# Kernel tuning notes

Hardware: AMD Instinct MI355X
Metric: run time of the kernel (lower is better)

The kernel has to match this reference:

```python
import jax, jax.numpy as jnp
import numpy as np

B, T, C = 1, 2048, 1024
E = 32            # n_routed_experts
TOPK = 4
H = 512           # expert_hidden_size
HS = 1024         # shared hidden: round_up(2*512, 256)
ROUTE_SCALE = 1.0


def setup_inputs() -> dict:
    key = jax.random.key(0)
    ks = jax.random.split(key, 6)
    s = 0.02  # init scale for stable logits/activations
    return {
        "x": jax.random.normal(ks[0], (B, T, C), jnp.float32),
        "gate_w": jax.random.normal(ks[1], (C, E), jnp.float32) * s,
        "gate_bias": jnp.zeros((E,), jnp.float32),
        "shared_gate_w": jax.random.normal(ks[2], (C, 2 * HS), jnp.float32) * s,
        "shared_down_w": jax.random.normal(ks[3], (HS, C), jnp.float32) * s,
        "expert_gate_w": jax.random.normal(ks[4], (E, C, 2 * H), jnp.float32) * s,
        "expert_down_w": jax.random.normal(ks[5], (E, H, C), jnp.float32) * s,
    }


def _swiglu(x, gate_w, down_w):
    # torch: y, gate = chunk(gate_proj(x), 2); down(silu(gate) * y)
    u = x @ gate_w
    y, g = jnp.split(u, 2, axis=-1)
    return (jax.nn.silu(g) * y) @ down_w


def reference(x, gate_w, gate_bias, shared_gate_w, shared_down_w,
              expert_gate_w, expert_down_w):
    Bx, Tx, Cx = x.shape
    xf = x.reshape(-1, Cx)                     # (N, C)
    N = xf.shape[0]

    # shared expert (always active)
    shared = _swiglu(x, shared_gate_w, shared_down_w)   # (B, T, C)

    # sigmoid top-k gate with load-balance bias (bias only affects selection)
    scores = jax.nn.sigmoid(xf @ gate_w)                # (N, E)
    _, topk_idx = jax.lax.top_k(scores + gate_bias, TOPK)
    w = jnp.take_along_axis(scores, topk_idx, axis=-1)  # (N, K)
    w = w / jnp.sum(w, axis=-1, keepdims=True) * ROUTE_SCALE

    # dense combine weights: combine[n, e] = routing weight of expert e for token n (0 if unselected)
    combine = jnp.zeros((N, E), xf.dtype).at[jnp.arange(N)[:, None], topk_idx].add(w)

    # routed experts: masked dense evaluation (math identical to permute + grouped GEMM + scatter-combine)
    out = jnp.zeros_like(xf)
    for e in range(E):
        out = out + combine[:, e:e + 1] * _swiglu(xf, expert_gate_w[e], expert_down_w[e])

    return shared + out.reshape(Bx, Tx, Cx)
```

## Files before the change

### kernel.cpp

```cpp
#include <hip/hip_runtime.h>
#include <hip/hip_bf16.h>
#include <math.h>

#define N_TOK 2048
#define C_DIM 1024
#define E_NUM 32
#define TOPKK 4
#define H_EXP 512
#define HS_SH 1024
#define NSLOT (N_TOK * TOPKK)

typedef __attribute__((ext_vector_type(8))) short short8;
typedef __attribute__((ext_vector_type(4))) float f32x4;

__device__ __forceinline__ ushort f2b(float f) {
    __hip_bfloat16 h = __float2bfloat16(f);
    return *(ushort*)&h;
}
__device__ __forceinline__ float silu_f(float g) { return g / (1.f + __expf(-g)); }

__device__ __forceinline__ void glds16(const ushort* g, ushort* l) {
    __builtin_amdgcn_global_load_lds(
        (const __attribute__((address_space(1))) unsigned int*)g,
        (__attribute__((address_space(3))) unsigned int*)l, 16, 0, 0);
}

__device__ __forceinline__ void router_body(
    int n, int t, const float* __restrict__ x, const float* __restrict__ gate_w,
    const float* __restrict__ gate_bias, ushort* __restrict__ xb,
    int* __restrict__ topk_idx, float* __restrict__ topk_w, char* smem)
{
    float* xs = (float*)smem;
    float (*part)[E_NUM] = (float(*)[E_NUM])(smem + 4096);
    float* scores_s = (float*)(smem + 4096 + 1024);
    const float* xr = x + (size_t)n * C_DIM;
    {
        float4 v = ((const float4*)xr)[t];
        xs[t * 4 + 0] = v.x; xs[t * 4 + 1] = v.y;
        xs[t * 4 + 2] = v.z; xs[t * 4 + 3] = v.w;
        ushort4 o;
        o.x = f2b(v.x); o.y = f2b(v.y); o.z = f2b(v.z); o.w = f2b(v.w);
        ((ushort4*)(xb + (size_t)n * C_DIM))[t] = o;
    }
    __syncthreads();
    const int e = t & 31, cp = t >> 5;
    float s = 0.f;
#pragma unroll 4
    for (int c = cp * 128; c < cp * 128 + 128; ++c)
        s += xs[c] * gate_w[c * E_NUM + e];
    part[cp][e] = s;
    __syncthreads();
    if (t < E_NUM) {
        float tot = 0.f;
#pragma unroll
        for (int i = 0; i < 8; ++i) tot += part[i][t];
        scores_s[t] = 1.f / (1.f + expf(-tot));
    }
    __syncthreads();
    if (t < 64) {
        const int l = t;
        const float sc  = (l < E_NUM) ? scores_s[l] : -INFINITY;
        const float scb = (l < E_NUM) ? sc + gate_bias[l] : -INFINITY;
        bool used = false;
        int myidx[TOPKK]; float myw[TOPKK]; float wsum = 0.f;
#pragma unroll
        for (int k = 0; k < TOPKK; ++k) {
            float v = used ? -INFINITY : scb;
            float m = v;
#pragma unroll
            for (int d = 1; d < 64; d <<= 1) m = fmaxf(m, __shfl_xor(m, d));
            unsigned long long b = __ballot(v == m);
            const int pick = __ffsll((unsigned long long)b) - 1;
            if (l == pick) used = true;
            const float w = __shfl(sc, pick);
            myidx[k] = pick; myw[k] = w; wsum += w;
        }
        if (l == 0) {
            const float inv = 1.0f / wsum;
#pragma unroll
            for (int k = 0; k < TOPKK; ++k) {
                topk_idx[n * TOPKK + k] = myidx[k];
                topk_w[n * TOPKK + k] = myw[k] * inv;
            }
        }
    }
}

template<int K, int N, int PAIR_H>
__device__ __forceinline__ void transp_body(const float* __restrict__ in,
                                            ushort* __restrict__ out,
                                            int bx, int by, int bz, int t, char* smem)
{
    const float* inp = in + (size_t)bz * K * N;
    ushort* outp = out + (size_t)bz * K * N;
    ushort (*T)[132] = (ushort(*)[132])smem;
    const int k0 = by * 64, n0 = bx * 128;
    {
        const int rr = t >> 5;
        const int c4 = (t & 31) * 4;
        float4 v[8];
#pragma unroll
        for (int i = 0; i < 8; ++i)
            v[i] = *(const float4*)(inp + (size_t)(k0 + rr + i * 8) * N + n0 + c4);
#pragma unroll
        for (int i = 0; i < 8; ++i) {
            const int row = rr + i * 8;
            ushort4 o;
            o.x = f2b(v[i].x); o.y = f2b(v[i].y); o.z = f2b(v[i].z); o.w = f2b(v[i].w);
            *(ushort4*)&T[row][c4 ^ ((row >> 3) << 2)] = o;
        }
    }
    __syncthreads();
    {
        const int g  = t >> 3;
        const int kg = t & 7;
#pragma unroll
        for (int p = 0; p < 4; ++p) {
            const int nn = p * 32 + g;
            const int nsw = nn ^ (kg << 2);
            const int gn = n0 + nn;
            int np;
            if (PAIR_H > 0)
                np = (gn < PAIR_H) ? ((gn >> 4) * 32 + (gn & 15))
                                   : (((gn - PAIR_H) >> 4) * 32 + 16 + ((gn - PAIR_H) & 15));
            else
                np = gn;
            short8 o;
#pragma unroll
            for (int j = 0; j < 8; ++j) o[j] = (short)T[kg * 8 + j][nsw];
            *(short8*)(outp + (size_t)np * K + k0 + kg * 8) = o;
        }
    }
}

__global__ __launch_bounds__(256) void prep_mega(
    const float* __restrict__ x, const float* __restrict__ gw,
    const float* __restrict__ gb, const float* __restrict__ sgw,
    const float* __restrict__ egw, ushort* __restrict__ xb,
    int* __restrict__ topk_idx, float* __restrict__ topk_w,
    ushort* __restrict__ sgw_t, ushort* __restrict__ egw_t)
{
    __shared__ __align__(16) char smem[16896];
    const int b = blockIdx.x;
    const int t = threadIdx.x;
    if (b < 256) {
        transp_body<C_DIM, 2 * HS_SH, HS_SH>(sgw, sgw_t, b & 15, b >> 4, 0, t, smem);
    } else if (b < 4352) {
        const int r = b - 256;
        transp_body<C_DIM, 2 * H_EXP, H_EXP>(egw, egw_t, r & 7, (r >> 3) & 15, r >> 7, t, smem);
    } else {
        router_body(b - 4352, t, x, gw, gb, xb, topk_idx, topk_w, smem);
    }
}

__global__ __launch_bounds__(1024) void route_build(
    const int* __restrict__ topk_idx, const float* __restrict__ topk_w,
    int* __restrict__ offsets, int* __restrict__ perm_token,
    float* __restrict__ perm_w, int* __restrict__ inv_slot)
{
    __shared__ int cnt[E_NUM];
    __shared__ int off_s[E_NUM + 1];
    const int t = threadIdx.x;
    if (t < E_NUM) cnt[t] = 0;
    __syncthreads();
    int myidx[8];
#pragma unroll
    for (int j = 0; j < 8; ++j) {
        const int i = t * 8 + j;
        myidx[j] = topk_idx[i];
        atomicAdd(&cnt[myidx[j]], 1);
    }
    __syncthreads();
    if (t == 0) {
        int a = 0;
        for (int e2 = 0; e2 < E_NUM; ++e2) { off_s[e2] = a; a += cnt[e2]; }
        off_s[E_NUM] = a;
    }
    __syncthreads();
    if (t < E_NUM) cnt[t] = off_s[t];
    if (t <= E_NUM) offsets[t] = off_s[t];
    __syncthreads();
#pragma unroll
    for (int j = 0; j < 8; ++j) {
        const int i = t * 8 + j;
        const int pos = atomicAdd(&cnt[myidx[j]], 1);
        perm_token[pos] = i >> 2;
        perm_w[pos] = topk_w[i];
        inv_slot[i] = pos;
    }
}

template<int K, int NP, bool EXPERT>
__device__ __forceinline__ void swiglu_body(
    const ushort* __restrict__ Ab, const ushort* __restrict__ Bt,
    ushort* __restrict__ Out, const int* __restrict__ offsets,
    const int* __restrict__ perm_tok, int eidx, ushort* S)
{
    constexpr int H = NP / 2;
    int base = 0, cnt = N_TOK;
    const ushort* Bp = Bt;
    if (EXPERT) {
        base = offsets[eidx]; cnt = offsets[eidx + 1] - base;
        Bp = Bt + (size_t)eidx * NP * K;
    }
    const int n0 = blockIdx.x * 128;
    if (n0 >= NP) return;
    const int m0 = blockIdx.y * 128;
    if (m0 >= cnt) return;
    ushort* O = Out + (size_t)base * H;

    ushort* As = S;
    ushort* Bs = S + 128 * 64;

    const int t = threadIdx.x;
    const int lane = t & 63, wave = t >> 6;
    const int wr = wave >> 1, wc = wave & 1;
    const int quad = lane >> 4, l16 = lane & 15;
    const int srow = lane >> 3;
    const int schunk = (lane & 7) ^ srow;

    f32x4 acc[4][4];
#pragma unroll
    for (int i = 0; i < 4; ++i)
#pragma unroll
        for (int j = 0; j < 4; ++j) acc[i][j] = (f32x4){0.f, 0.f, 0.f, 0.f};

    const ushort* AgI[4];
#pragma unroll
    for (int i = 0; i < 4; ++i) {
        int ar = m0 + wave * 8 + srow + i * 32;
        if (EXPERT) {
            ar = ar < cnt ? ar : 0;
            AgI[i] = Ab + (size_t)perm_tok[base + ar] * K + schunk * 8;
        } else {
            AgI[i] = Ab + (size_t)(base + ar) * K + schunk * 8;
        }
    }
    const ushort* Bg = Bp + (size_t)(n0 + wave * 8 + srow) * K + schunk * 8;

    for (int k0 = 0; k0 < K; k0 += 64) {
        __syncthreads();
#pragma unroll
        for (int i = 0; i < 4; ++i) {
            glds16(AgI[i] + k0, As + (wave * 8 + i * 32) * 64);
            glds16(Bg + (size_t)(i * 32) * K + k0, Bs + (wave * 8 + i * 32) * 64);
        }
        __syncthreads();
#pragma unroll
        for (int ks = 0; ks < 2; ++ks) {
            const int coff = (((ks * 4 + quad) ^ (l16 & 7)) << 3);
            short8 af[4], bfr[4];
#pragma unroll
            for (int i = 0; i < 4; ++i) {
                af[i]  = *(const short8*)(As + (wr * 64 + i * 16 + l16) * 64 + coff);
                bfr[i] = *(const short8*)(Bs + (wc * 64 + i * 16 + l16) * 64 + coff);
            }
#pragma unroll
            for (int tm = 0; tm < 4; ++tm)
#pragma unroll
                for (int tn = 0; tn < 4; ++tn)
                    acc[tm][tn] = __builtin_amdgcn_mfma_f32_16x16x32_bf16(
                        af[tm], bfr[tn], acc[tm][tn], 0, 0, 0);
        }
    }

    __syncthreads();
#pragma unroll
    for (int tm = 0; tm < 4; ++tm)
#pragma unroll
        for (int p = 0; p < 2; ++p)
#pragma unroll
            for (int r = 0; r < 4; ++r) {
                const int ml = wr * 64 + tm * 16 + quad * 4 + r;
                const int hl = wc * 32 + p * 16 + l16;
                const float y = acc[tm][2 * p][r];
                const float g = acc[tm][2 * p + 1][r];
                S[ml * 72 + hl] = f2b(silu_f(g) * y);
            }
    __syncthreads();
#pragma unroll
    for (int i = 0; i < 4; ++i) {
        const int c = t + i * 256;
        const int row = c >> 3, col = (c & 7) * 8;
        if (m0 + row < cnt)
            *(float4*)(O + (size_t)(m0 + row) * H + (n0 >> 1) + col) =
                *(const float4*)(S + row * 72 + col);
    }
}

template<int K, bool EXPERT>
__device__ __forceinline__ void down_body(
    const ushort* __restrict__ Ab, const ushort* __restrict__ Bt,
    float* __restrict__ Out, const int* __restrict__ offsets,
    const float* __restrict__ perm_w, int eidx, ushort* S)
{
    int base = 0, cnt = N_TOK;
    const ushort* Bp = Bt;
    if (EXPERT) {
        base = offsets[eidx]; cnt = offsets[eidx + 1] - base;
        Bp = Bt + (size_t)eidx * C_DIM * K;
    }
    const int m0 = blockIdx.y * 128;
    if (m0 >= cnt) return;
    const int n0 = blockIdx.x * 128;
    const ushort* Ap = Ab + (size_t)base * K;

    ushort* As = S;
    ushort* Bs = S + 128 * 64;

    const int t = threadIdx.x;
    const int lane = t & 63, wave = t >> 6;
    const int wr = wave >> 1, wc = wave & 1;
    const int quad = lane >> 4, l16 = lane & 15;
    const int srow = lane >> 3;
    const int schunk = (lane & 7) ^ srow;

    f32x4 acc[4][4];
#pragma unroll
    for (int i = 0; i < 4; ++i)
#pragma unroll
        for (int j = 0; j < 4; ++j) acc[i][j] = (f32x4){0.f, 0.f, 0.f, 0.f};

    const ushort* Ag = Ap + (size_t)(m0 + wave * 8 + srow) * K + schunk * 8;
    const ushort* Bg = Bp + (size_t)(n0 + wave * 8 + srow) * K + schunk * 8;

    for (int k0 = 0; k0 < K; k0 += 64) {
        __syncthreads();
#pragma unroll
        for (int i = 0; i < 4; ++i) {
            glds16(Ag + (size_t)(i * 32) * K + k0, As + (wave * 8 + i * 32) * 64);
            glds16(Bg + (size_t)(i * 32) * K + k0, Bs + (wave * 8 + i * 32) * 64);
        }
        __syncthreads();
#pragma unroll
        for (int ks = 0; ks < 2; ++ks) {
            const int coff = (((ks * 4 + quad) ^ (l16 & 7)) << 3);
            short8 af[4], bfr[4];
#pragma unroll
            for (int i = 0; i < 4; ++i) {
                af[i]  = *(const short8*)(As + (wr * 64 + i * 16 + l16) * 64 + coff);
                bfr[i] = *(const short8*)(Bs + (wc * 64 + i * 16 + l16) * 64 + coff);
            }
#pragma unroll
            for (int tm = 0; tm < 4; ++tm)
#pragma unroll
                for (int tn = 0; tn < 4; ++tn)
                    acc[tm][tn] = __builtin_amdgcn_mfma_f32_16x16x32_bf16(
                        af[tm], bfr[tn], acc[tm][tn], 0, 0, 0);
        }
    }

#pragma unroll
    for (int tm = 0; tm < 4; ++tm)
#pragma unroll
        for (int r = 0; r < 4; ++r) {
            const int grow = m0 + wr * 64 + tm * 16 + quad * 4 + r;
            if (EXPERT) {
                if (grow < cnt) {
                    const float w = perm_w[base + grow];
#pragma unroll
                    for (int tn = 0; tn < 4; ++tn) {
                        const int col = n0 + wc * 64 + tn * 16 + l16;
                        Out[(size_t)(base + grow) * C_DIM + col] = w * acc[tm][tn][r];
                    }
                }
            } else {
#pragma unroll
                for (int tn = 0; tn < 4; ++tn) {
                    const int col = n0 + wc * 64 + tn * 16 + l16;
                    Out[(size_t)grow * C_DIM + col] = acc[tm][tn][r];
                }
            }
        }
}

__global__ __launch_bounds__(256, 3) void swiglu_fused(
    const ushort* __restrict__ xb, const ushort* __restrict__ sgw_t,
    const ushort* __restrict__ egw_t, ushort* __restrict__ Hs_b,
    ushort* __restrict__ He_b, const int* __restrict__ offsets,
    const int* __restrict__ perm_tok,
    const float* __restrict__ sdw, const float* __restrict__ edw,
    ushort* __restrict__ sdw_t, ushort* __restrict__ edw_t)
{
    __shared__ __align__(16) ushort S[2 * 128 * 64];
    const int z = blockIdx.z;
    if (z >= 33) {
        const int flat = (z - 33) * 256 + blockIdx.y * 16 + blockIdx.x;
        if (flat < 128) {
            transp_body<HS_SH, C_DIM, 0>(sdw, sdw_t, flat & 7, flat >> 3, 0,
                                         threadIdx.x, (char*)S);
        } else if (flat < 2176) {
            const int r = flat - 128;
            transp_body<H_EXP, C_DIM, 0>(edw, edw_t, r & 7, (r >> 3) & 7, r >> 6,
                                         threadIdx.x, (char*)S);
        }
        return;
    }
    if (z < E_NUM)
        swiglu_body<C_DIM, 2 * H_EXP, true>(xb, egw_t, He_b, offsets, perm_tok, z, S);
    else
        swiglu_body<C_DIM, 2 * HS_SH, false>(xb, sgw_t, Hs_b, nullptr, nullptr, 0, S);
}

__global__ __launch_bounds__(256, 3) void down_fused(
    const ushort* __restrict__ Hs_b, const ushort* __restrict__ He_b,
    const ushort* __restrict__ sdw_t, const ushort* __restrict__ edw_t,
    float* __restrict__ out, float* __restrict__ Ye,
    const int* __restrict__ offsets, const float* __restrict__ perm_w)
{
    __shared__ __align__(16) ushort S[2 * 128 * 64];
    const int z = blockIdx.z;
    if (z < E_NUM)
        down_body<H_EXP, true>(He_b, edw_t, Ye, offsets, perm_w, z, S);
    else
        down_body<HS_SH, false>(Hs_b, sdw_t, out, nullptr, nullptr, 0, S);
}

__global__ __launch_bounds__(256) void combine_kernel(
    const float* __restrict__ Ye, const int* __restrict__ inv_slot,
    float* __restrict__ Out)
{
    const int tok = blockIdx.x;
    __shared__ int s4[TOPKK];
    if (threadIdx.x < TOPKK) s4[threadIdx.x] = inv_slot[tok * TOPKK + threadIdx.x];
    __syncthreads();
    const int c = threadIdx.x * 4;
    float4 acc = *(const float4*)(Out + (size_t)tok * C_DIM + c);
#pragma unroll
    for (int k = 0; k < TOPKK; ++k) {
        float4 v = *(const float4*)(Ye + (size_t)s4[k] * C_DIM + c);
        acc.x += v.x; acc.y += v.y; acc.z += v.z; acc.w += v.w;
    }
    *(float4*)(Out + (size_t)tok * C_DIM + c) = acc;
}

extern "C" void kernel_launch(void* const* d_in, const int* in_sizes, int n_in,
                              void* d_out, int out_size, void* d_ws, size_t ws_size,
                              hipStream_t stream)
{
    const float* x   = (const float*)d_in[0];
    const float* gw  = (const float*)d_in[1];
    const float* gb  = (const float*)d_in[2];
    const float* sgw = (const float*)d_in[3];
    const float* sdw = (const float*)d_in[4];
    const float* egw = (const float*)d_in[5];
    const float* edw = (const float*)d_in[6];
    float* out = (float*)d_out;

    char* ws = (char*)d_ws;
    size_t off = 0;
    auto alloc = [&](size_t bytes) -> void* {
        void* p = ws + off;
        off = (off + bytes + 255) & ~(size_t)255;
        return p;
    };
    int*    topk_idx = (int*)   alloc((size_t)NSLOT * sizeof(int));
    float*  topk_w   = (float*) alloc((size_t)NSLOT * sizeof(float));
    int*    offsets  = (int*)   alloc((E_NUM + 1) * sizeof(int));
    int*    perm_tok = (int*)   alloc((size_t)NSLOT * sizeof(int));
    float*  perm_w   = (float*) alloc((size_t)NSLOT * sizeof(float));
    int*    inv_slot = (int*)   alloc((size_t)NSLOT * sizeof(int));
    ushort* xb       = (ushort*)alloc((size_t)N_TOK * C_DIM * 2);
    ushort* sgw_t    = (ushort*)alloc((size_t)C_DIM * 2 * HS_SH * 2);
    ushort* sdw_t    = (ushort*)alloc((size_t)HS_SH * C_DIM * 2);
    ushort* egw_t    = (ushort*)alloc((size_t)E_NUM * C_DIM * 2 * H_EXP * 2);
    ushort* edw_t    = (ushort*)alloc((size_t)E_NUM * H_EXP * C_DIM * 2);
    ushort* Hs_b     = (ushort*)alloc((size_t)N_TOK * HS_SH * 2);
    ushort* He_b     = (ushort*)alloc((size_t)(NSLOT + 128) * H_EXP * 2);
    float*  Ye       = (float*) alloc((size_t)(NSLOT + 128) * C_DIM * sizeof(float));
    (void)ws_size; (void)in_sizes; (void)n_in; (void)out_size;

    prep_mega<<<6400, 256, 0, stream>>>(x, gw, gb, sgw, egw,
                                        xb, topk_idx, topk_w, sgw_t, egw_t);
    route_build<<<1, 1024, 0, stream>>>(topk_idx, topk_w, offsets, perm_tok, perm_w, inv_slot);
    swiglu_fused<<<dim3(16, N_TOK / 128, 42), 256, 0, stream>>>(
        xb, sgw_t, egw_t, Hs_b, He_b, offsets, perm_tok, sdw, edw, sdw_t, edw_t);
    down_fused<<<dim3(C_DIM / 128, N_TOK / 128, E_NUM + 1), 256, 0, stream>>>(
        Hs_b, He_b, sdw_t, edw_t, out, Ye, offsets, perm_w);
    combine_kernel<<<N_TOK, 256, 0, stream>>>(Ye, inv_slot, out);
}
```

Baseline: 379.6 us.

## Reschedule weight transposes to overlap with GEMM phases across kernels

Splits the prep/swiglu/down kernels into phases so each weight transpose (expert gate, shared down, expert down) runs in the same launch as an independent GEMM: shared swiglu overlaps expert-gate transpose, expert swiglu overlaps shared down and expert-down transpose. Grids are flattened to 1D with explicit block coordinates. The aim is to hide memory-bound transposes behind compute-bound GEMMs and shorten the critical path, at the cost of one extra kernel launch and a changed block mix per launch.

```diff
diff --git a/kernel.cpp b/kernel.cpp
--- a/kernel.cpp
+++ b/kernel.cpp
@@ -133,24 +133,19 @@
     }
 }
 
-__global__ __launch_bounds__(256) void prep_mega(
+__global__ __launch_bounds__(256) void prep1(
     const float* __restrict__ x, const float* __restrict__ gw,
     const float* __restrict__ gb, const float* __restrict__ sgw,
-    const float* __restrict__ egw, ushort* __restrict__ xb,
-    int* __restrict__ topk_idx, float* __restrict__ topk_w,
-    ushort* __restrict__ sgw_t, ushort* __restrict__ egw_t)
+    ushort* __restrict__ xb, int* __restrict__ topk_idx,
+    float* __restrict__ topk_w, ushort* __restrict__ sgw_t)
 {
     __shared__ __align__(16) char smem[16896];
     const int b = blockIdx.x;
     const int t = threadIdx.x;
-    if (b < 256) {
+    if (b < 256)
         transp_body<C_DIM, 2 * HS_SH, HS_SH>(sgw, sgw_t, b & 15, b >> 4, 0, t, smem);
-    } else if (b < 4352) {
-        const int r = b - 256;
-        transp_body<C_DIM, 2 * H_EXP, H_EXP>(egw, egw_t, r & 7, (r >> 3) & 15, r >> 7, t, smem);
-    } else {
-        router_body(b - 4352, t, x, gw, gb, xb, topk_idx, topk_w, smem);
-    }
+    else
+        router_body(b - 256, t, x, gw, gb, xb, topk_idx, topk_w, smem);
 }
 
 __global__ __launch_bounds__(1024) void route_build(
@@ -194,7 +189,7 @@
 __device__ __forceinline__ void swiglu_body(
     const ushort* __restrict__ Ab, const ushort* __restrict__ Bt,
     ushort* __restrict__ Out, const int* __restrict__ offsets,
-    const int* __restrict__ perm_tok, int eidx, ushort* S)
+    const int* __restrict__ perm_tok, int eidx, int bx, int by, ushort* S)
 {
     constexpr int H = NP / 2;
     int base = 0, cnt = N_TOK;
@@ -203,9 +198,8 @@
         base = offsets[eidx]; cnt = offsets[eidx + 1] - base;
         Bp = Bt + (size_t)eidx * NP * K;
     }
-    const int n0 = blockIdx.x * 128;
-    if (n0 >= NP) return;
-    const int m0 = blockIdx.y * 128;
+    const int n0 = bx * 128;
+    const int m0 = by * 128;
     if (m0 >= cnt) return;
     ushort* O = Out + (size_t)base * H;
 
@@ -292,7 +286,7 @@
 __device__ __forceinline__ void down_body(
     const ushort* __restrict__ Ab, const ushort* __restrict__ Bt,
     float* __restrict__ Out, const int* __restrict__ offsets,
-    const float* __restrict__ perm_w, int eidx, ushort* S)
+    const float* __restrict__ perm_w, int eidx, int bx, int by, ushort* S)
 {
     int base = 0, cnt = N_TOK;
     const ushort* Bp = Bt;
@@ -300,9 +294,9 @@
         base = offsets[eidx]; cnt = offsets[eidx + 1] - base;
         Bp = Bt + (size_t)eidx * C_DIM * K;
     }
-    const int m0 = blockIdx.y * 128;
+    const int m0 = by * 128;
     if (m0 >= cnt) return;
-    const int n0 = blockIdx.x * 128;
+    const int n0 = bx * 128;
     const ushort* Ap = Ab + (size_t)base * K;
 
     ushort* As = S;
@@ -374,46 +368,63 @@
         }
 }
 
-__global__ __launch_bounds__(256, 3) void swiglu_fused(
+__global__ __launch_bounds__(256, 3) void phase3(
     const ushort* __restrict__ xb, const ushort* __restrict__ sgw_t,
-    const ushort* __restrict__ egw_t, ushort* __restrict__ Hs_b,
+    ushort* __restrict__ Hs_b, const float* __restrict__ egw,
+    const float* __restrict__ sdw, ushort* __restrict__ egw_t,
+    ushort* __restrict__ sdw_t)
+{
+    __shared__ __align__(16) ushort S[2 * 128 * 64];
+    const int b = blockIdx.x;
+    const int t = threadIdx.x;
+    if (b < 256) {
+        swiglu_body<C_DIM, 2 * HS_SH, false>(xb, sgw_t, Hs_b, nullptr, nullptr, 0,
+                                             b & 15, b >> 4, S);
+    } else if (b < 4352) {
+        const int r = b - 256;
+        transp_body<C_DIM, 2 * H_EXP, H_EXP>(egw, egw_t, r & 7, (r >> 3) & 15, r >> 7,
+                                             t, (char*)S);
+    } else {
+        const int r = b - 4352;
+        transp_body<HS_SH, C_DIM, 0>(sdw, sdw_t, r & 7, r >> 3, 0, t, (char*)S);
+    }
+}
+
+__global__ __launch_bounds__(256, 3) void phase4(
+    const ushort* __restrict__ xb, const ushort* __restrict__ egw_t,
     ushort* __restrict__ He_b, const int* __restrict__ offsets,
-    const int* __restrict__ perm_tok,
-    const float* __restrict__ sdw, const float* __restrict__ edw,
-    ushort* __restrict__ sdw_t, ushort* __restrict__ edw_t)
+    const int* __restrict__ perm_tok, const ushort* __restrict__ Hs_b,
+    const ushort* __restrict__ sdw_t, float* __restrict__ out,
+    const float* __restrict__ edw, ushort* __restrict__ edw_t)
 {
     __shared__ __align__(16) ushort S[2 * 128 * 64];
-    const int z = blockIdx.z;
-    if (z >= 33) {
-        const int flat = (z - 33) * 256 + blockIdx.y * 16 + blockIdx.x;
-        if (flat < 128) {
-            transp_body<HS_SH, C_DIM, 0>(sdw, sdw_t, flat & 7, flat >> 3, 0,
-                                         threadIdx.x, (char*)S);
-        } else if (flat < 2176) {
-            const int r = flat - 128;
-            transp_body<H_EXP, C_DIM, 0>(edw, edw_t, r & 7, (r >> 3) & 7, r >> 6,
-                                         threadIdx.x, (char*)S);
-        }
-        return;
-    }
-    if (z < E_NUM)
-        swiglu_body<C_DIM, 2 * H_EXP, true>(xb, egw_t, He_b, offsets, perm_tok, z, S);
-    else
-        swiglu_body<C_DIM, 2 * HS_SH, false>(xb, sgw_t, Hs_b, nullptr, nullptr, 0, S);
-}
-
-__global__ __launch_bounds__(256, 3) void down_fused(
-    const ushort* __restrict__ Hs_b, const ushort* __restrict__ He_b,
-    const ushort* __restrict__ sdw_t, const ushort* __restrict__ edw_t,
-    float* __restrict__ out, float* __restrict__ Ye,
-    const int* __restrict__ offsets, const float* __restrict__ perm_w)
+    const int b = blockIdx.x;
+    const int t = threadIdx.x;
+    if (b < 4096) {
+        const int r = b & 127;
+        swiglu_body<C_DIM, 2 * H_EXP, true>(xb, egw_t, He_b, offsets, perm_tok,
+                                            b >> 7, r & 7, r >> 3, S);
+    } else if (b < 4224) {
+        const int r = b - 4096;
+        down_body<HS_SH, false>(Hs_b, sdw_t, out, nullptr, nullptr, 0,
+                                r & 7, r >> 3, S);
+    } else {
+        const int r = b - 4224;
+        transp_body<H_EXP, C_DIM, 0>(edw, edw_t, r & 7, (r >> 3) & 7, r >> 6,
+                                     t, (char*)S);
+    }
+}
+
+__global__ __launch_bounds__(256, 3) void phase5(
+    const ushort* __restrict__ He_b, const ushort* __restrict__ edw_t,
+    float* __restrict__ Ye, const int* __restrict__ offsets,
+    const float* __restrict__ perm_w)
 {
     __shared__ __align__(16) ushort S[2 * 128 * 64];
-    const int z = blockIdx.z;
-    if (z < E_NUM)
-        down_body<H_EXP, true>(He_b, edw_t, Ye, offsets, perm_w, z, S);
-    else
-        down_body<HS_SH, false>(Hs_b, sdw_t, out, nullptr, nullptr, 0, S);
+    const int b = blockIdx.x;
+    const int r = b & 127;
+    down_body<H_EXP, true>(He_b, edw_t, Ye, offsets, perm_w, b >> 7,
+                           r & 7, r >> 3, S);
 }
 
 __global__ __launch_bounds__(256) void combine_kernel(
@@ -470,12 +481,11 @@
     float*  Ye       = (float*) alloc((size_t)(NSLOT + 128) * C_DIM * sizeof(float));
     (void)ws_size; (void)in_sizes; (void)n_in; (void)out_size;
 
-    prep_mega<<<6400, 256, 0, stream>>>(x, gw, gb, sgw, egw,
-                                        xb, topk_idx, topk_w, sgw_t, egw_t);
+    prep1<<<2304, 256, 0, stream>>>(x, gw, gb, sgw, xb, topk_idx, topk_w, sgw_t);
     route_build<<<1, 1024, 0, stream>>>(topk_idx, topk_w, offsets, perm_tok, perm_w, inv_slot);
-    swiglu_fused<<<dim3(16, N_TOK / 128, 42), 256, 0, stream>>>(
-        xb, sgw_t, egw_t, Hs_b, He_b, offsets, perm_tok, sdw, edw, sdw_t, edw_t);
-    down_fused<<<dim3(C_DIM / 128, N_TOK / 128, E_NUM + 1), 256, 0, stream>>>(
-        Hs_b, He_b, sdw_t, edw_t, out, Ye, offsets, perm_w);
+    phase3<<<4480, 256, 0, stream>>>(xb, sgw_t, Hs_b, egw, sdw, egw_t, sdw_t);
+    phase4<<<6272, 256, 0, stream>>>(xb, egw_t, He_b, offsets, perm_tok,
+                                     Hs_b, sdw_t, out, edw, edw_t);
+    phase5<<<4096, 256, 0, stream>>>(He_b, edw_t, Ye, offsets, perm_w);
     combine_kernel<<<N_TOK, 256, 0, stream>>>(Ye, inv_slot, out);
 }
```

Measured after the change: 354.2 us. -6.7%, faster.
